# Optimization experiments

Hardware: AMD Instinct MI355X
Metric: run time of the kernel (lower is better)

The kernel has to match this reference:

```python
import jax, jax.numpy as jnp
import numpy as np

N, E, H, R = 32768, 524288, 128, 64
INV_SQRT_3 = 1.0 / np.sqrt(3.0)
INV_SQRT_H = 1.0 / np.sqrt(float(H))
INV_SQRT_2 = 1.0 / np.sqrt(2.0)


def scaled_silu(x):
    return jax.nn.silu(x) * (1.0 / 0.6)


def setup_inputs() -> dict:
    key = jax.random.key(0)
    ks = jax.random.split(key, 16)
    s = 0.05
    return {
        "x": jax.random.normal(ks[0], (N, H), jnp.float32),
        "vec": jax.random.normal(ks[1], (N, 3, H), jnp.float32),
        "edge_index": jax.random.randint(ks[2], (2, E), 0, N),
        "edge_embed": jax.random.normal(ks[3], (E, R), jnp.float32),
        "edge_vec": jax.random.normal(ks[4], (E, 3), jnp.float32),
        # message layer params
        "ln_g": jnp.ones((H,), jnp.float32),
        "ln_b": jnp.zeros((H,), jnp.float32),
        "W1": jax.random.normal(ks[5], (H, H), jnp.float32) * s,
        "b1": jnp.zeros((H,), jnp.float32),
        "W2": jax.random.normal(ks[6], (H, 3 * H), jnp.float32) * s,
        "b2": jnp.zeros((3 * H,), jnp.float32),
        "Wr": jax.random.normal(ks[7], (R, 3 * H), jnp.float32) * s,
        "br": jnp.zeros((3 * H,), jnp.float32),
        # update layer params
        "Wv": jax.random.normal(ks[8], (H, 2 * H), jnp.float32) * s,
        "Wu1": jax.random.normal(ks[9], (2 * H, H), jnp.float32) * s,
        "bu1": jnp.zeros((H,), jnp.float32),
        "Wu2": jax.random.normal(ks[10], (H, 3 * H), jnp.float32) * s,
        "bu2": jnp.zeros((3 * H,), jnp.float32),
    }


def _layernorm(x, g, b, eps=1e-5):
    mu = jnp.mean(x, axis=-1, keepdims=True)
    var = jnp.mean((x - mu) ** 2, axis=-1, keepdims=True)
    return (x - mu) * jax.lax.rsqrt(var + eps) * g + b


def _painn(x, vec, edge_index, edge_embed, edge_vec,
           ln_g, ln_b, W1, b1, W2, b2, Wr, br, Wv, Wu1, bu1, Wu2, bu2):
    src, dst = edge_index[0], edge_index[1]
    # --- message ---
    xh = scaled_silu(_layernorm(x, ln_g, ln_b) @ W1 + b1) @ W2 + b2  # [N,3H]
    rbfh = edge_embed @ Wr + br                                       # [E,3H]
    m = xh[src] * rbfh                                                # [E,3H]
    xh1, xh2, xh3 = jnp.split(m, 3, axis=-1)
    xh2 = xh2 * INV_SQRT_3
    vec_msg = (vec[src] * xh2[:, None, :] + xh3[:, None, :] * edge_vec[:, :, None]) * INV_SQRT_H  # [E,3,H]
    dx = jax.ops.segment_sum(xh1, dst, num_segments=N)
    dvec = jax.ops.segment_sum(vec_msg, dst, num_segments=N)
    x = (x + dx) * INV_SQRT_2
    vec = vec + dvec
    # --- update ---
    vproj = jnp.einsum('nch,hk->nck', vec, Wv)  # [N,3,2H]
    vec1, vec2 = jnp.split(vproj, 2, axis=-1)
    vec_dot = jnp.sum(vec1 * vec2, axis=1) * INV_SQRT_H  # [N,H]
    vec2_norm = jnp.sqrt(jnp.sum(vec2 ** 2, axis=-2) + 1e-8)  # [N,H]
    h = scaled_silu(jnp.concatenate([x, vec2_norm], axis=-1) @ Wu1 + bu1) @ Wu2 + bu2
    xv1, xv2, xv3 = jnp.split(h, 3, axis=-1)
    dx = (xv1 + xv2 * vec_dot) * INV_SQRT_2
    dvec = xv3[:, None, :] * vec1
    return vec + dvec, x + dx


def reference(x, vec, edge_index, edge_embed, edge_vec,
              ln_g, ln_b, W1, b1, W2, b2, Wr, br, Wv, Wu1, bu1, Wu2, bu2):
    return _painn(x, vec, edge_index, edge_embed, edge_vec,
                  ln_g, ln_b, W1, b1, W2, b2, Wr, br, Wv, Wu1, bu1, Wu2, bu2)
```

## Files before the change

kernel.cpp:

```cpp
#include <hip/hip_runtime.h>
#include <cstdint>
#include <cstddef>

#define NN 32768
#define NE 524288
#define H  128
#define H3 384
#define RB 64
#define EB 16
#define NPB 4
#define EEST 72
#define MSTRIDE 388
#define AST 136

#define INV_SQRT_3 0.5773502691896258f
#define INV_SQRT_H 0.08838834764831845f
#define INV_SQRT_2 0.7071067811865476f

typedef __attribute__((ext_vector_type(8))) short short8;
typedef __attribute__((ext_vector_type(4))) float f32x4;

__device__ __forceinline__ float scaled_silu(float v) {
    return v * (1.0f / 0.6f) / (1.0f + __expf(-v));
}
__device__ __forceinline__ short f2bf(float f) {
    uint32_t u = __float_as_uint(f);
    uint32_t r = (u + 0x7FFFu + ((u >> 16) & 1u)) >> 16;
    return (short)r;
}
__device__ __forceinline__ float bf2f(short s) {
    return __uint_as_float(((uint32_t)(uint16_t)s) << 16);
}

__global__ __launch_bounds__(256) void cvtT_kernel(const float* __restrict__ W,
        short* __restrict__ WT, int K, int M) {
    int i = blockIdx.x * 256 + threadIdx.x;
    int k = i / M, m = i % M;
    WT[(size_t)m * K + k] = f2bf(W[(size_t)k * M + m]);
}

__global__ __launch_bounds__(256) void veccvt_kernel(const float* __restrict__ v,
        short* __restrict__ vb) {
    int i = blockIdx.x * 256 + threadIdx.x;
    float4 a = ((const float4*)v)[i];
    short4 s4; s4.x = f2bf(a.x); s4.y = f2bf(a.y); s4.z = f2bf(a.z); s4.w = f2bf(a.w);
    ((short4*)vb)[i] = s4;
}

__global__ __launch_bounds__(256) void ln_kernel(const float* __restrict__ x,
        const float* __restrict__ g, const float* __restrict__ b,
        float* __restrict__ t) {
    int row  = blockIdx.x * 4 + (threadIdx.x >> 6);
    int lane = threadIdx.x & 63;
    const float* xr = x + (size_t)row * H;
    float v0 = xr[lane], v1 = xr[lane + 64];
    float s = v0 + v1;
#pragma unroll
    for (int off = 32; off; off >>= 1) s += __shfl_xor(s, off, 64);
    float mu = s * (1.0f / 128.0f);
    float d0 = v0 - mu, d1 = v1 - mu;
    float q = d0 * d0 + d1 * d1;
#pragma unroll
    for (int off = 32; off; off >>= 1) q += __shfl_xor(q, off, 64);
    float rs = rsqrtf(q * (1.0f / 128.0f) + 1e-5f);
    float* tr = t + (size_t)row * H;
    tr[lane]      = d0 * rs * g[lane]      + b[lane];
    tr[lane + 64] = d1 * rs * g[lane + 64] + b[lane + 64];
}

__global__ __launch_bounds__(256) void g1_mfma(const float* __restrict__ t,
        const short* __restrict__ W1T, const float* __restrict__ b1,
        short* __restrict__ h1_bf) {
    __shared__ short A_l[64 * AST];
    __shared__ short B_l[128 * AST];
    int tid = threadIdx.x;
    int w = tid >> 6, l = tid & 63, lm = l & 15, q = l >> 4;
    int r0 = blockIdx.x * 64;
    const float4* ag = (const float4*)(t + (size_t)r0 * H);
#pragma unroll
    for (int i = 0; i < 8; ++i) {
        int idx = tid + 256 * i;
        float4 a = ag[idx];
        int row = idx >> 5, c4 = idx & 31;
        short4 s4; s4.x = f2bf(a.x); s4.y = f2bf(a.y); s4.z = f2bf(a.z); s4.w = f2bf(a.w);
        *(short4*)&A_l[row * AST + c4 * 4] = s4;
    }
    const short8* wg = (const short8*)W1T;
#pragma unroll
    for (int i = 0; i < 8; ++i) {
        int idx = tid + 256 * i;
        int row = idx >> 4, c8 = idx & 15;
        *(short8*)&B_l[row * AST + c8 * 8] = wg[idx];
    }
    __syncthreads();
    short8 bf[2][4];
#pragma unroll
    for (int c = 0; c < 2; ++c)
#pragma unroll
        for (int ks = 0; ks < 4; ++ks)
            bf[c][ks] = *(const short8*)&B_l[((2 * w + c) * 16 + lm) * AST + ks * 32 + q * 8];
    f32x4 acc[4][2];
#pragma unroll
    for (int rt = 0; rt < 4; ++rt) { acc[rt][0] = (f32x4){0.f,0.f,0.f,0.f}; acc[rt][1] = (f32x4){0.f,0.f,0.f,0.f}; }
#pragma unroll
    for (int ks = 0; ks < 4; ++ks)
#pragma unroll
        for (int rt = 0; rt < 4; ++rt) {
            short8 a = *(const short8*)&A_l[(rt * 16 + lm) * AST + ks * 32 + q * 8];
            acc[rt][0] = __builtin_amdgcn_mfma_f32_16x16x32_bf16(a, bf[0][ks], acc[rt][0], 0, 0, 0);
            acc[rt][1] = __builtin_amdgcn_mfma_f32_16x16x32_bf16(a, bf[1][ks], acc[rt][1], 0, 0, 0);
        }
#pragma unroll
    for (int c = 0; c < 2; ++c) {
        int col = (2 * w + c) * 16 + lm;
        float bb = b1[col];
#pragma unroll
        for (int rt = 0; rt < 4; ++rt)
#pragma unroll
            for (int r = 0; r < 4; ++r) {
                int R = r0 + rt * 16 + q * 4 + r;
                h1_bf[(size_t)R * H + col] = f2bf(scaled_silu(acc[rt][c][r] + bb));
            }
    }
}

__global__ __launch_bounds__(256) void g2_mfma(const short* __restrict__ h1_bf,
        const short* __restrict__ W2T, const float* __restrict__ b2,
        short* __restrict__ xh_bf) {
    __shared__ short A_l[64 * AST];
    __shared__ short B_l[128 * AST];
    int tid = threadIdx.x;
    int w = tid >> 6, l = tid & 63, lm = l & 15, q = l >> 4;
    int r0 = blockIdx.x * 64;
    const short8* ag = (const short8*)(h1_bf + (size_t)r0 * H);
#pragma unroll
    for (int i = 0; i < 4; ++i) {
        int idx = tid + 256 * i;
        int row = idx >> 4, c8 = idx & 15;
        *(short8*)&A_l[row * AST + c8 * 8] = ag[idx];
    }
    for (int s = 0; s < 3; ++s) {
        __syncthreads();
        const short8* wg = (const short8*)(W2T + (size_t)s * 128 * 128);
#pragma unroll
        for (int i = 0; i < 8; ++i) {
            int idx = tid + 256 * i;
            int row = idx >> 4, c8 = idx & 15;
            *(short8*)&B_l[row * AST + c8 * 8] = wg[idx];
        }
        __syncthreads();
        short8 bf[2][4];
#pragma unroll
        for (int c = 0; c < 2; ++c)
#pragma unroll
            for (int ks = 0; ks < 4; ++ks)
                bf[c][ks] = *(const short8*)&B_l[((2 * w + c) * 16 + lm) * AST + ks * 32 + q * 8];
        f32x4 acc[4][2];
#pragma unroll
        for (int rt = 0; rt < 4; ++rt) { acc[rt][0] = (f32x4){0.f,0.f,0.f,0.f}; acc[rt][1] = (f32x4){0.f,0.f,0.f,0.f}; }
#pragma unroll
        for (int ks = 0; ks < 4; ++ks)
#pragma unroll
            for (int rt = 0; rt < 4; ++rt) {
                short8 a = *(const short8*)&A_l[(rt * 16 + lm) * AST + ks * 32 + q * 8];
                acc[rt][0] = __builtin_amdgcn_mfma_f32_16x16x32_bf16(a, bf[0][ks], acc[rt][0], 0, 0, 0);
                acc[rt][1] = __builtin_amdgcn_mfma_f32_16x16x32_bf16(a, bf[1][ks], acc[rt][1], 0, 0, 0);
            }
#pragma unroll
        for (int c = 0; c < 2; ++c) {
            int col = (2 * w + c) * 16 + lm;
            float bb = b2[s * H + col];
#pragma unroll
            for (int rt = 0; rt < 4; ++rt)
#pragma unroll
                for (int r = 0; r < 4; ++r) {
                    int R = r0 + rt * 16 + q * 4 + r;
                    xh_bf[(size_t)R * H3 + s * H + col] = f2bf(acc[rt][c][r] + bb);
                }
        }
    }
}

__global__ __launch_bounds__(256) void hist_kernel(const int* __restrict__ eidx,
        int* __restrict__ hist) {
    int e = blockIdx.x * 256 + threadIdx.x;
    atomicAdd(&hist[eidx[NE + e]], 1);
}

__global__ __launch_bounds__(1024) void scan_kernel(const int* __restrict__ hist,
        int* __restrict__ row_ptr, int* __restrict__ cursor) {
    __shared__ int sc[1024];
    int t = threadIdx.x;
    int base = t * 32;
    int v[32];
    int s = 0;
#pragma unroll
    for (int i = 0; i < 32; ++i) {
        int tmp = hist[base + i];
        v[i] = s;
        s += tmp;
    }
    sc[t] = s;
    __syncthreads();
    for (int off = 1; off < 1024; off <<= 1) {
        int a = sc[t];
        int b = (t >= off) ? sc[t - off] : 0;
        __syncthreads();
        sc[t] = a + b;
        __syncthreads();
    }
    int excl = sc[t] - s;
#pragma unroll
    for (int i = 0; i < 32; ++i) {
        int val = excl + v[i];
        row_ptr[base + i] = val;
        cursor[base + i] = val;
    }
    if (t == 0) row_ptr[32768] = NE;
}

__global__ __launch_bounds__(256) void scatter_kernel(const int* __restrict__ eidx,
        const float* __restrict__ evec, int* __restrict__ cursor,
        int* __restrict__ perm, int* __restrict__ srcs_s, int* __restrict__ dsts_s,
        float* __restrict__ ev_s) {
    int e = blockIdx.x * 256 + threadIdx.x;
    int d = eidx[NE + e];
    int pos = atomicAdd(&cursor[d], 1);
    perm[pos]   = e;
    srcs_s[pos] = eidx[e];
    dsts_s[pos] = d;
    ev_s[pos * 3 + 0] = evec[e * 3 + 0];
    ev_s[pos * 3 + 1] = evec[e * 3 + 1];
    ev_s[pos * 3 + 2] = evec[e * 3 + 2];
}

__global__ __launch_bounds__(256) void eegather_kernel(const int* __restrict__ perm,
        const float* __restrict__ eembed, short* __restrict__ ee_s) {
    int idx = blockIdx.x * 256 + threadIdx.x;
    int pos = idx >> 3, t = idx & 7;
    int e = perm[pos];
    const float4* src = (const float4*)(eembed + (size_t)e * RB);
    float4 a = src[t * 2];
    float4 b = src[t * 2 + 1];
    short8 s;
    s[0] = f2bf(a.x); s[1] = f2bf(a.y); s[2] = f2bf(a.z); s[3] = f2bf(a.w);
    s[4] = f2bf(b.x); s[5] = f2bf(b.y); s[6] = f2bf(b.z); s[7] = f2bf(b.w);
    ((short8*)(ee_s + (size_t)pos * RB))[t] = s;
}

__global__ __launch_bounds__(256) void wrt_kernel(const float* __restrict__ Wr,
        short* __restrict__ WrT16) {
    int i = blockIdx.x * 256 + threadIdx.x;
    int n = i >> 6, k = i & 63;
    WrT16[i] = f2bf(Wr[(size_t)k * H3 + n]);
}

__global__ __launch_bounds__(384) void edge_mfma_kernel(
        const int* __restrict__ row_ptr,
        const int* __restrict__ srcs_s, const int* __restrict__ dsts_s,
        const float* __restrict__ ev_s, const short* __restrict__ ee_s,
        const short* __restrict__ WrT16, const float* __restrict__ br,
        const short* __restrict__ xh_bf, const short* __restrict__ vec_bf,
        const float* __restrict__ xin, const float* __restrict__ vecin,
        float* __restrict__ dx_out, float* __restrict__ dvec_out) {
    __shared__ float accdx[NPB * H];
    __shared__ float accdv[NPB * H3];
    __shared__ short eeL[EB * EEST];
    __shared__ float mst[EB * MSTRIDE];
    __shared__ int   sSrc[EB];
    __shared__ int   sLd[EB];
    __shared__ float sEv[EB][3];
    int j = threadIdx.x;
    int w = j >> 6, l = j & 63;
    int lm = l & 15, q = l >> 4;
    short8 bfrag[4][2];
#pragma unroll
    for (int t = 0; t < 4; ++t)
#pragma unroll
        for (int hf = 0; hf < 2; ++hf)
            bfrag[t][hf] = *(const short8*)(WrT16 +
                ((size_t)(w * 64 + t * 16 + lm) * 64 + q * 8 + hf * 32));
    float brj[4];
#pragma unroll
    for (int t = 0; t < 4; ++t) brj[t] = br[w * 64 + t * 16 + lm];
    float scale = (w < 2) ? 1.0f : ((w < 4) ? (INV_SQRT_3 * INV_SQRT_H) : INV_SQRT_H);
    int n0 = blockIdx.x * NPB;
    for (int i = j; i < NPB * H;  i += 384) accdx[i] = 0.f;
    for (int i = j; i < NPB * H3; i += 384) accdv[i] = 0.f;
    int ib = row_ptr[n0], ie = row_ptr[n0 + NPB];
    int c = j >> 7, hh = j & 127;
    __syncthreads();
    for (int base = ib; base < ie; base += EB) {
        int cnt = min(EB, ie - base);
        if (j < 128) {
            int e = j >> 3, c8 = j & 7;
            int i = base + ((e < cnt) ? e : 0);
            *(short8*)(eeL + e * EEST + c8 * 8) =
                ((const short8*)ee_s)[(size_t)i * 8 + c8];
        }
        if (j < EB) {
            int i = base + ((j < cnt) ? j : 0);
            sSrc[j] = srcs_s[i];
            sLd[j]  = dsts_s[i] - n0;
            sEv[j][0] = ev_s[(size_t)i * 3 + 0];
            sEv[j][1] = ev_s[(size_t)i * 3 + 1];
            sEv[j][2] = ev_s[(size_t)i * 3 + 2];
        }
        __syncthreads();
        short xg[4][4];
#pragma unroll
        for (int r = 0; r < 4; ++r) {
            const short* xr = xh_bf + (size_t)sSrc[q * 4 + r] * H3 + w * 64 + lm;
#pragma unroll
            for (int t = 0; t < 4; ++t) xg[r][t] = xr[t * 16];
        }
        short vv[EB];
#pragma unroll
        for (int e = 0; e < EB; ++e)
            vv[e] = vec_bf[(size_t)sSrc[e] * H3 + j];
        short8 a0 = *(const short8*)(eeL + lm * EEST + q * 8);
        short8 a1 = *(const short8*)(eeL + lm * EEST + 32 + q * 8);
        f32x4 d[4];
#pragma unroll
        for (int t = 0; t < 4; ++t) {
            d[t] = __builtin_amdgcn_mfma_f32_16x16x32_bf16(a0, bfrag[t][0],
                       (f32x4){0.f, 0.f, 0.f, 0.f}, 0, 0, 0);
            d[t] = __builtin_amdgcn_mfma_f32_16x16x32_bf16(a1, bfrag[t][1], d[t], 0, 0, 0);
        }
#pragma unroll
        for (int r = 0; r < 4; ++r) {
            int e = q * 4 + r;
#pragma unroll
            for (int t = 0; t < 4; ++t) {
                float m = (d[t][r] + brj[t]) * bf2f(xg[r][t]) * scale;
                mst[e * MSTRIDE + w * 64 + t * 16 + lm] = m;
            }
        }
        __syncthreads();
        int cur = -1; float dva = 0.f, dxa = 0.f;
#pragma unroll
        for (int e = 0; e < EB; ++e) {
            if (e < cnt) {
                float m2 = mst[e * MSTRIDE + H + hh];
                float m3 = mst[e * MSTRIDE + 2 * H + hh];
                int ld = sLd[e];
                if (ld != cur) {
                    if (cur >= 0) {
                        accdv[cur * H3 + j] += dva;
                        if (j < H) accdx[cur * H + j] += dxa;
                    }
                    cur = ld; dva = 0.f; dxa = 0.f;
                }
                dva += bf2f(vv[e]) * m2 + m3 * sEv[e][c];
                if (j < H) dxa += mst[e * MSTRIDE + j];
            }
        }
        if (cur >= 0) {
            accdv[cur * H3 + j] += dva;
            if (j < H) accdx[cur * H + j] += dxa;
        }
        __syncthreads();
    }
    for (int i = j; i < NPB * H;  i += 384)
        dx_out[(size_t)n0 * H + i] = (xin[(size_t)n0 * H + i] + accdx[i]) * INV_SQRT_2;
    for (int i = j; i < NPB * H3; i += 384)
        dvec_out[(size_t)n0 * H3 + i] = vecin[(size_t)n0 * H3 + i] + accdv[i];
}

__global__ __launch_bounds__(256) void d1_vproj(const float* __restrict__ vec_mid,
        const short* __restrict__ WvT, float* __restrict__ vec1,
        float* __restrict__ vdot, short* __restrict__ vnorm_bf) {
    __shared__ short A_l[48 * AST];
    __shared__ short B_l[128 * AST];
    __shared__ float T1[48 * 132];
    __shared__ float T2[48 * 132];
    int tid = threadIdx.x;
    int w = tid >> 6, l = tid & 63, lm = l & 15, q = l >> 4;
    int r0 = blockIdx.x * 48;
    const float4* ag = (const float4*)(vec_mid + (size_t)r0 * H);
#pragma unroll
    for (int i = 0; i < 6; ++i) {
        int idx = tid + 256 * i;
        float4 a = ag[idx];
        int row = idx >> 5, c4 = idx & 31;
        short4 s4; s4.x = f2bf(a.x); s4.y = f2bf(a.y); s4.z = f2bf(a.z); s4.w = f2bf(a.w);
        *(short4*)&A_l[row * AST + c4 * 4] = s4;
    }
    for (int s = 0; s < 2; ++s) {
        __syncthreads();
        const short8* wg = (const short8*)(WvT + (size_t)s * 128 * 128);
#pragma unroll
        for (int i = 0; i < 8; ++i) {
            int idx = tid + 256 * i;
            int row = idx >> 4, c8 = idx & 15;
            *(short8*)&B_l[row * AST + c8 * 8] = wg[idx];
        }
        __syncthreads();
        short8 bf[2][4];
#pragma unroll
        for (int c = 0; c < 2; ++c)
#pragma unroll
            for (int ks = 0; ks < 4; ++ks)
                bf[c][ks] = *(const short8*)&B_l[((2 * w + c) * 16 + lm) * AST + ks * 32 + q * 8];
        f32x4 acc[3][2];
#pragma unroll
        for (int rt = 0; rt < 3; ++rt) { acc[rt][0] = (f32x4){0.f,0.f,0.f,0.f}; acc[rt][1] = (f32x4){0.f,0.f,0.f,0.f}; }
#pragma unroll
        for (int ks = 0; ks < 4; ++ks)
#pragma unroll
            for (int rt = 0; rt < 3; ++rt) {
                short8 a = *(const short8*)&A_l[(rt * 16 + lm) * AST + ks * 32 + q * 8];
                acc[rt][0] = __builtin_amdgcn_mfma_f32_16x16x32_bf16(a, bf[0][ks], acc[rt][0], 0, 0, 0);
                acc[rt][1] = __builtin_amdgcn_mfma_f32_16x16x32_bf16(a, bf[1][ks], acc[rt][1], 0, 0, 0);
            }
        float* T = s ? T2 : T1;
#pragma unroll
        for (int c = 0; c < 2; ++c) {
            int col = (2 * w + c) * 16 + lm;
#pragma unroll
            for (int rt = 0; rt < 3; ++rt)
#pragma unroll
                for (int r = 0; r < 4; ++r) {
                    int lr = rt * 16 + q * 4 + r;
                    float v = acc[rt][c][r];
                    T[lr * 132 + col] = v;
                    if (s == 0) vec1[(size_t)(r0 + lr) * H + col] = v;
                }
        }
    }
    __syncthreads();
    int nb = blockIdx.x * 16;
#pragma unroll
    for (int i = 0; i < 8; ++i) {
        int p = tid + 256 * i;
        int k = p & 127, m = p >> 7;
        float d = 0.f, s2 = 0.f;
#pragma unroll
        for (int c = 0; c < 3; ++c) {
            float v1 = T1[(m * 3 + c) * 132 + k];
            float v2 = T2[(m * 3 + c) * 132 + k];
            d += v1 * v2; s2 += v2 * v2;
        }
        vdot[(size_t)(nb + m) * H + k] = d * INV_SQRT_H;
        vnorm_bf[(size_t)(nb + m) * H + k] = f2bf(sqrtf(s2 + 1e-8f));
    }
}

__global__ __launch_bounds__(256) void d2a_mfma(const float* __restrict__ xmid,
        const short* __restrict__ vnorm_bf, const short* __restrict__ Wu1T,
        const float* __restrict__ bu1, short* __restrict__ u_bf) {
    __shared__ short A_l[64 * AST];
    __shared__ short B_l[128 * AST];
    int tid = threadIdx.x;
    int w = tid >> 6, l = tid & 63, lm = l & 15, q = l >> 4;
    int r0 = blockIdx.x * 64;
    f32x4 acc[4][2];
#pragma unroll
    for (int rt = 0; rt < 4; ++rt) { acc[rt][0] = (f32x4){0.f,0.f,0.f,0.f}; acc[rt][1] = (f32x4){0.f,0.f,0.f,0.f}; }
    for (int kh = 0; kh < 2; ++kh) {
        __syncthreads();
        if (kh == 0) {
            const float4* ag = (const float4*)(xmid + (size_t)r0 * H);
#pragma unroll
            for (int i = 0; i < 8; ++i) {
                int idx = tid + 256 * i;
                float4 a = ag[idx];
                int row = idx >> 5, c4 = idx & 31;
                short4 s4; s4.x = f2bf(a.x); s4.y = f2bf(a.y); s4.z = f2bf(a.z); s4.w = f2bf(a.w);
                *(short4*)&A_l[row * AST + c4 * 4] = s4;
            }
        } else {
            const short8* ag = (const short8*)(vnorm_bf + (size_t)r0 * H);
#pragma unroll
            for (int i = 0; i < 4; ++i) {
                int idx = tid + 256 * i;
                int row = idx >> 4, c8 = idx & 15;
                *(short8*)&A_l[row * AST + c8 * 8] = ag[idx];
            }
        }
#pragma unroll
        for (int i = 0; i < 8; ++i) {
            int idx = tid + 256 * i;
            int row = idx >> 4, c8 = idx & 15;
            *(short8*)&B_l[row * AST + c8 * 8] = ((const short8*)Wu1T)[row * 32 + kh * 16 + c8];
        }
        __syncthreads();
        short8 bf[2][4];
#pragma unroll
        for (int c = 0; c < 2; ++c)
#pragma unroll
            for (int ks = 0; ks < 4; ++ks)
                bf[c][ks] = *(const short8*)&B_l[((2 * w + c) * 16 + lm) * AST + ks * 32 + q * 8];
#pragma unroll
        for (int ks = 0; ks < 4; ++ks)
#pragma unroll
            for (int rt = 0; rt < 4; ++rt) {
                short8 a = *(const short8*)&A_l[(rt * 16 + lm) * AST + ks * 32 + q * 8];
                acc[rt][0] = __builtin_amdgcn_mfma_f32_16x16x32_bf16(a, bf[0][ks], acc[rt][0], 0, 0, 0);
                acc[rt][1] = __builtin_amdgcn_mfma_f32_16x16x32_bf16(a, bf[1][ks], acc[rt][1], 0, 0, 0);
            }
    }
#pragma unroll
    for (int c = 0; c < 2; ++c) {
        int col = (2 * w + c) * 16 + lm;
        float bb = bu1[col];
#pragma unroll
        for (int rt = 0; rt < 4; ++rt)
#pragma unroll
            for (int r = 0; r < 4; ++r) {
                int R = r0 + rt * 16 + q * 4 + r;
                u_bf[(size_t)R * H + col] = f2bf(scaled_silu(acc[rt][c][r] + bb));
            }
    }
}

__global__ __launch_bounds__(256) void d2b_mfma(const short* __restrict__ u_bf,
        const short* __restrict__ Wu2T, const float* __restrict__ bu2,
        const float* __restrict__ vdot, const float* __restrict__ xmid,
        const float* __restrict__ vec_mid, const float* __restrict__ vec1,
        float* __restrict__ out) {
    __shared__ short A_l[64 * AST];
    __shared__ short B_l[128 * AST];
    int tid = threadIdx.x;
    int w = tid >> 6, l = tid & 63, lm = l & 15, q = l >> 4;
    int r0 = blockIdx.x * 64;
    float* out_vec = out;
    float* out_x = out + (size_t)NN * H3;
    const short8* ag = (const short8*)(u_bf + (size_t)r0 * H);
#pragma unroll
    for (int i = 0; i < 4; ++i) {
        int idx = tid + 256 * i;
        int row = idx >> 4, c8 = idx & 15;
        *(short8*)&A_l[row * AST + c8 * 8] = ag[idx];
    }
    short8 bf0[2][4], bf1[2][4];
    __syncthreads();
    {
        const short8* wg = (const short8*)Wu2T;
#pragma unroll
        for (int i = 0; i < 8; ++i) {
            int idx = tid + 256 * i;
            int row = idx >> 4, c8 = idx & 15;
            *(short8*)&B_l[row * AST + c8 * 8] = wg[idx];
        }
    }
    __syncthreads();
#pragma unroll
    for (int c = 0; c < 2; ++c)
#pragma unroll
        for (int ks = 0; ks < 4; ++ks)
            bf0[c][ks] = *(const short8*)&B_l[((2 * w + c) * 16 + lm) * AST + ks * 32 + q * 8];
    __syncthreads();
    {
        const short8* wg = (const short8*)(Wu2T + 128 * 128);
#pragma unroll
        for (int i = 0; i < 8; ++i) {
            int idx = tid + 256 * i;
            int row = idx >> 4, c8 = idx & 15;
            *(short8*)&B_l[row * AST + c8 * 8] = wg[idx];
        }
    }
    __syncthreads();
#pragma unroll
    for (int c = 0; c < 2; ++c)
#pragma unroll
        for (int ks = 0; ks < 4; ++ks)
            bf1[c][ks] = *(const short8*)&B_l[((2 * w + c) * 16 + lm) * AST + ks * 32 + q * 8];
    f32x4 acc0[4][2], acc1[4][2];
#pragma unroll
    for (int rt = 0; rt < 4; ++rt) {
        acc0[rt][0] = (f32x4){0.f,0.f,0.f,0.f}; acc0[rt][1] = (f32x4){0.f,0.f,0.f,0.f};
        acc1[rt][0] = (f32x4){0.f,0.f,0.f,0.f}; acc1[rt][1] = (f32x4){0.f,0.f,0.f,0.f};
    }
#pragma unroll
    for (int ks = 0; ks < 4; ++ks)
#pragma unroll
        for (int rt = 0; rt < 4; ++rt) {
            short8 a = *(const short8*)&A_l[(rt * 16 + lm) * AST + ks * 32 + q * 8];
            acc0[rt][0] = __builtin_amdgcn_mfma_f32_16x16x32_bf16(a, bf0[0][ks], acc0[rt][0], 0, 0, 0);
            acc0[rt][1] = __builtin_amdgcn_mfma_f32_16x16x32_bf16(a, bf0[1][ks], acc0[rt][1], 0, 0, 0);
            acc1[rt][0] = __builtin_amdgcn_mfma_f32_16x16x32_bf16(a, bf1[0][ks], acc1[rt][0], 0, 0, 0);
            acc1[rt][1] = __builtin_amdgcn_mfma_f32_16x16x32_bf16(a, bf1[1][ks], acc1[rt][1], 0, 0, 0);
        }
#pragma unroll
    for (int c = 0; c < 2; ++c) {
        int col = (2 * w + c) * 16 + lm;
        float bb0 = bu2[col], bb1 = bu2[H + col];
#pragma unroll
        for (int rt = 0; rt < 4; ++rt)
#pragma unroll
            for (int r = 0; r < 4; ++r) {
                int R = r0 + rt * 16 + q * 4 + r;
                float xv1 = acc0[rt][c][r] + bb0;
                float xv2 = acc1[rt][c][r] + bb1;
                float dx2 = (xv1 + xv2 * vdot[(size_t)R * H + col]) * INV_SQRT_2;
                out_x[(size_t)R * H + col] = xmid[(size_t)R * H + col] + dx2;
            }
    }
    __syncthreads();
    {
        const short8* wg = (const short8*)(Wu2T + 2 * 128 * 128);
#pragma unroll
        for (int i = 0; i < 8; ++i) {
            int idx = tid + 256 * i;
            int row = idx >> 4, c8 = idx & 15;
            *(short8*)&B_l[row * AST + c8 * 8] = wg[idx];
        }
    }
    __syncthreads();
#pragma unroll
    for (int c = 0; c < 2; ++c)
#pragma unroll
        for (int ks = 0; ks < 4; ++ks)
            bf0[c][ks] = *(const short8*)&B_l[((2 * w + c) * 16 + lm) * AST + ks * 32 + q * 8];
#pragma unroll
    for (int rt = 0; rt < 4; ++rt) { acc0[rt][0] = (f32x4){0.f,0.f,0.f,0.f}; acc0[rt][1] = (f32x4){0.f,0.f,0.f,0.f}; }
#pragma unroll
    for (int ks = 0; ks < 4; ++ks)
#pragma unroll
        for (int rt = 0; rt < 4; ++rt) {
            short8 a = *(const short8*)&A_l[(rt * 16 + lm) * AST + ks * 32 + q * 8];
            acc0[rt][0] = __builtin_amdgcn_mfma_f32_16x16x32_bf16(a, bf0[0][ks], acc0[rt][0], 0, 0, 0);
            acc0[rt][1] = __builtin_amdgcn_mfma_f32_16x16x32_bf16(a, bf0[1][ks], acc0[rt][1], 0, 0, 0);
        }
#pragma unroll
    for (int c = 0; c < 2; ++c) {
        int col = (2 * w + c) * 16 + lm;
        float bb2 = bu2[2 * H + col];
#pragma unroll
        for (int rt = 0; rt < 4; ++rt)
#pragma unroll
            for (int r = 0; r < 4; ++r) {
                int R = r0 + rt * 16 + q * 4 + r;
                float xv3 = acc0[rt][c][r] + bb2;
#pragma unroll
                for (int c3 = 0; c3 < 3; ++c3) {
                    size_t idx = (size_t)R * H3 + c3 * H + col;
                    out_vec[idx] = vec_mid[idx] + xv3 * vec1[idx];
                }
            }
    }
}

extern "C" void kernel_launch(void* const* d_in, const int* in_sizes, int n_in,
                              void* d_out, int out_size, void* d_ws, size_t ws_size,
                              hipStream_t stream) {
    const float* x    = (const float*)d_in[0];
    const float* vec  = (const float*)d_in[1];
    const int*   eidx = (const int*)d_in[2];
    const float* eemb = (const float*)d_in[3];
    const float* evec = (const float*)d_in[4];
    const float* lng  = (const float*)d_in[5];
    const float* lnb  = (const float*)d_in[6];
    const float* W1   = (const float*)d_in[7];
    const float* b1   = (const float*)d_in[8];
    const float* W2   = (const float*)d_in[9];
    const float* b2   = (const float*)d_in[10];
    const float* Wr   = (const float*)d_in[11];
    const float* br   = (const float*)d_in[12];
    const float* Wv   = (const float*)d_in[13];
    const float* Wu1  = (const float*)d_in[14];
    const float* bu1  = (const float*)d_in[15];
    const float* Wu2  = (const float*)d_in[16];
    const float* bu2  = (const float*)d_in[17];

    float* B0 = (float*)d_ws;
    float* B1 = B0 + (size_t)NN * H3;
    float* B2 = B1 + (size_t)NN * H3;
    float* B3 = B2 + (size_t)NN * H;
    float* B4 = B3 + (size_t)NN * H;
    short* B5 = (short*)(B4 + (size_t)NN * H);
    float* out = (float*)d_out;
    short* ee_s = (short*)d_out;

    int* row_ptr = (int*)B4;
    int* cursor  = row_ptr + 32772;
    int* perm    = cursor + 32768;
    int* srcs_s  = perm + NE;
    int* dsts_s  = srcs_s + NE;
    float* ev_s  = (float*)(dsts_s + NE);
    short* WrT16 = (short*)(ev_s + (size_t)NE * 3);

    short* vec_bf = B5;
    short* W1T  = vec_bf + (size_t)NN * H3;
    short* W2T  = W1T + 128 * 128;
    short* WvT  = W2T + 128 * 384;
    short* Wu1T = WvT + 128 * 256;
    short* Wu2T = Wu1T + 256 * 128;

    short* xh_bf    = (short*)B0;
    short* h1_bf    = (short*)B3;
    short* vnorm_bf = (short*)B4;
    short* u_bf     = vnorm_bf + (size_t)NN * H;

    cvtT_kernel<<<64,  256, 0, stream>>>(W1,  W1T,  128, 128);
    cvtT_kernel<<<192, 256, 0, stream>>>(W2,  W2T,  128, 384);
    cvtT_kernel<<<128, 256, 0, stream>>>(Wv,  WvT,  128, 256);
    cvtT_kernel<<<128, 256, 0, stream>>>(Wu1, Wu1T, 256, 128);
    cvtT_kernel<<<192, 256, 0, stream>>>(Wu2, Wu2T, 128, 384);
    wrt_kernel<<<(H3 * RB) / 256, 256, 0, stream>>>(Wr, WrT16);
    veccvt_kernel<<<(NN * H3 / 4) / 256, 256, 0, stream>>>(vec, vec_bf);

    ln_kernel<<<NN / 4, 256, 0, stream>>>(x, lng, lnb, B2);
    g1_mfma<<<NN / 64, 256, 0, stream>>>(B2, W1T, b1, h1_bf);
    g2_mfma<<<NN / 64, 256, 0, stream>>>(h1_bf, W2T, b2, xh_bf);

    hipMemsetAsync(row_ptr, 0, 32768 * sizeof(int), stream);
    hist_kernel<<<NE / 256, 256, 0, stream>>>(eidx, row_ptr);
    scan_kernel<<<1, 1024, 0, stream>>>(row_ptr, row_ptr, cursor);
    scatter_kernel<<<NE / 256, 256, 0, stream>>>(eidx, evec, cursor, perm, srcs_s, dsts_s, ev_s);
    eegather_kernel<<<(NE * 8) / 256, 256, 0, stream>>>(perm, eemb, ee_s);

    edge_mfma_kernel<<<NN / NPB, 384, 0, stream>>>(row_ptr, srcs_s, dsts_s, ev_s,
                                                   ee_s, WrT16, br, xh_bf, vec_bf,
                                                   x, vec, B2, B1);

    d1_vproj<<<(NN * 3) / 48, 256, 0, stream>>>(B1, WvT, B0, B3, vnorm_bf);
    d2a_mfma<<<NN / 64, 256, 0, stream>>>(B2, vnorm_bf, Wu1T, bu1, u_bf);
    d2b_mfma<<<NN / 64, 256, 0, stream>>>(u_bf, Wu2T, bu2, B3, B2, B1, B0, out);
}
```

Before: 937.0 us.

## Double-buffer edge metadata prefetch in edge kernel and batch LDS reads

The edge kernel now prefetches the next chunk's edge embeddings, source/destination indices and edge vectors into registers while the current chunk computes. It writes them into a second LDS buffer at the end of the iteration, which removes one barrier per chunk. The scatter loop loads all message values for 8 edges at once before accumulating, so LDS reads are no longer serialized with the segment logic. A min-blocks-per-CU launch bound of 4 is added to push occupancy, which caps registers per thread and may cause spills given the extra prefetch registers.

Measured after the change: 871.5 us. -7.0%, faster.

```diff
diff --git a/kernel.cpp b/kernel.cpp
--- a/kernel.cpp
+++ b/kernel.cpp
@@ -255,7 +255,7 @@
     WrT16[i] = f2bf(Wr[(size_t)k * H3 + n]);
 }
 
-__global__ __launch_bounds__(384) void edge_mfma_kernel(
+__global__ __launch_bounds__(384, 4) void edge_mfma_kernel(
         const int* __restrict__ row_ptr,
         const int* __restrict__ srcs_s, const int* __restrict__ dsts_s,
         const float* __restrict__ ev_s, const short* __restrict__ ee_s,
@@ -265,11 +265,11 @@
         float* __restrict__ dx_out, float* __restrict__ dvec_out) {
     __shared__ float accdx[NPB * H];
     __shared__ float accdv[NPB * H3];
-    __shared__ short eeL[EB * EEST];
+    __shared__ short eeL[2][EB * EEST];
     __shared__ float mst[EB * MSTRIDE];
-    __shared__ int   sSrc[EB];
-    __shared__ int   sLd[EB];
-    __shared__ float sEv[EB][3];
+    __shared__ int   sSrc[2][EB];
+    __shared__ int   sLd[2][EB];
+    __shared__ float sEv[2][EB][3];
     int j = threadIdx.x;
     int w = j >> 6, l = j & 63;
     int lm = l & 15, q = l >> 4;
@@ -289,37 +289,62 @@
     for (int i = j; i < NPB * H3; i += 384) accdv[i] = 0.f;
     int ib = row_ptr[n0], ie = row_ptr[n0 + NPB];
     int c = j >> 7, hh = j & 127;
-    __syncthreads();
+
+    if (ib < ie) {
+        int cnt0 = min(EB, ie - ib);
+        if (j < 128) {
+            int e = j >> 3, c8 = j & 7;
+            int i = ib + ((e < cnt0) ? e : 0);
+            *(short8*)(eeL[0] + e * EEST + c8 * 8) =
+                ((const short8*)ee_s)[(size_t)i * 8 + c8];
+        }
+        if (j < EB) {
+            int i = ib + ((j < cnt0) ? j : 0);
+            sSrc[0][j] = srcs_s[i];
+            sLd[0][j]  = dsts_s[i] - n0;
+            sEv[0][j][0] = ev_s[(size_t)i * 3 + 0];
+            sEv[0][j][1] = ev_s[(size_t)i * 3 + 1];
+            sEv[0][j][2] = ev_s[(size_t)i * 3 + 2];
+        }
+    }
+
+    int bsel = 0;
     for (int base = ib; base < ie; base += EB) {
         int cnt = min(EB, ie - base);
-        if (j < 128) {
-            int e = j >> 3, c8 = j & 7;
-            int i = base + ((e < cnt) ? e : 0);
-            *(short8*)(eeL + e * EEST + c8 * 8) =
-                ((const short8*)ee_s)[(size_t)i * 8 + c8];
-        }
-        if (j < EB) {
-            int i = base + ((j < cnt) ? j : 0);
-            sSrc[j] = srcs_s[i];
-            sLd[j]  = dsts_s[i] - n0;
-            sEv[j][0] = ev_s[(size_t)i * 3 + 0];
-            sEv[j][1] = ev_s[(size_t)i * 3 + 1];
-            sEv[j][2] = ev_s[(size_t)i * 3 + 2];
-        }
-        __syncthreads();
+        __syncthreads();
+        int nbase = base + EB;
+        int hn = nbase < ie;
+        short8 ereg = {0,0,0,0,0,0,0,0};
+        int msrc = 0, mdst = n0; float me0 = 0.f, me1 = 0.f, me2 = 0.f;
+        if (hn) {
+            int cntn = min(EB, ie - nbase);
+            if (j < 128) {
+                int e = j >> 3, c8 = j & 7;
+                int i = nbase + ((e < cntn) ? e : 0);
+                ereg = ((const short8*)ee_s)[(size_t)i * 8 + c8];
+            }
+            if (j < EB) {
+                int i = nbase + ((j < cntn) ? j : 0);
+                msrc = srcs_s[i]; mdst = dsts_s[i];
+                me0 = ev_s[(size_t)i * 3 + 0];
+                me1 = ev_s[(size_t)i * 3 + 1];
+                me2 = ev_s[(size_t)i * 3 + 2];
+            }
+        }
         short xg[4][4];
 #pragma unroll
         for (int r = 0; r < 4; ++r) {
-            const short* xr = xh_bf + (size_t)sSrc[q * 4 + r] * H3 + w * 64 + lm;
+            const short* xr = xh_bf + (size_t)sSrc[bsel][q * 4 + r] * H3 + w * 64 + lm;
 #pragma unroll
             for (int t = 0; t < 4; ++t) xg[r][t] = xr[t * 16];
         }
         short vv[EB];
 #pragma unroll
         for (int e = 0; e < EB; ++e)
-            vv[e] = vec_bf[(size_t)sSrc[e] * H3 + j];
-        short8 a0 = *(const short8*)(eeL + lm * EEST + q * 8);
-        short8 a1 = *(const short8*)(eeL + lm * EEST + 32 + q * 8);
+            vv[e] = vec_bf[(size_t)sSrc[bsel][e] * H3 + j];
+        const short* eeC = eeL[bsel];
+        short8 a0 = *(const short8*)(eeC + lm * EEST + q * 8);
+        short8 a1 = *(const short8*)(eeC + lm * EEST + 32 + q * 8);
         f32x4 d[4];
 #pragma unroll
         for (int t = 0; t < 4; ++t) {
@@ -339,28 +364,53 @@
         __syncthreads();
         int cur = -1; float dva = 0.f, dxa = 0.f;
 #pragma unroll
-        for (int e = 0; e < EB; ++e) {
-            if (e < cnt) {
-                float m2 = mst[e * MSTRIDE + H + hh];
-                float m3 = mst[e * MSTRIDE + 2 * H + hh];
-                int ld = sLd[e];
-                if (ld != cur) {
-                    if (cur >= 0) {
-                        accdv[cur * H3 + j] += dva;
-                        if (j < H) accdx[cur * H + j] += dxa;
+        for (int half = 0; half < 2; ++half) {
+            float m1g[8], m2g[8], m3g[8], evg[8];
+            int ldg[8];
+#pragma unroll
+            for (int u = 0; u < 8; ++u) {
+                int e = half * 8 + u;
+                m1g[u] = mst[e * MSTRIDE + j];
+                m2g[u] = mst[e * MSTRIDE + H + hh];
+                m3g[u] = mst[e * MSTRIDE + 2 * H + hh];
+                evg[u] = sEv[bsel][e][c];
+                ldg[u] = sLd[bsel][e];
+            }
+#pragma unroll
+            for (int u = 0; u < 8; ++u) {
+                int e = half * 8 + u;
+                if (e < cnt) {
+                    int ld = ldg[u];
+                    if (ld != cur) {
+                        if (cur >= 0) {
+                            accdv[cur * H3 + j] += dva;
+                            if (j < H) accdx[cur * H + j] += dxa;
+                        }
+                        cur = ld; dva = 0.f; dxa = 0.f;
                     }
-                    cur = ld; dva = 0.f; dxa = 0.f;
+                    dva += bf2f(vv[e]) * m2g[u] + m3g[u] * evg[u];
+                    if (j < H) dxa += m1g[u];
                 }
-                dva += bf2f(vv[e]) * m2 + m3 * sEv[e][c];
-                if (j < H) dxa += mst[e * MSTRIDE + j];
             }
         }
         if (cur >= 0) {
             accdv[cur * H3 + j] += dva;
             if (j < H) accdx[cur * H + j] += dxa;
         }
-        __syncthreads();
-    }
+        if (hn) {
+            int nb = bsel ^ 1;
+            if (j < 128) {
+                int e = j >> 3, c8 = j & 7;
+                *(short8*)(eeL[nb] + e * EEST + c8 * 8) = ereg;
+            }
+            if (j < EB) {
+                sSrc[nb][j] = msrc; sLd[nb][j] = mdst - n0;
+                sEv[nb][j][0] = me0; sEv[nb][j][1] = me1; sEv[nb][j][2] = me2;
+            }
+        }
+        bsel ^= 1;
+    }
+    __syncthreads();
     for (int i = j; i < NPB * H;  i += 384)
         dx_out[(size_t)n0 * H + i] = (xin[(size_t)n0 * H + i] + accdx[i]) * INV_SQRT_2;
     for (int i = j; i < NPB * H3; i += 384)
```
